# Optimization experiments

Measured on AMD Instinct MI355X. Metric: run time of the kernel, lower is better.

## Reference

```python
import jax, jax.numpy as jnp
import numpy as np

B, D = 16384, 1024

def setup_inputs() -> dict:
    key = jax.random.key(0)
    k1, k2, k3, k4 = jax.random.split(key, 4)
    return {
        "mu_q": jax.random.normal(k1, (B, D), dtype=jnp.float32),
        "sigma_q": jax.random.normal(k2, (B, D), dtype=jnp.float32),
        "mu_p": jax.random.normal(k3, (B, D), dtype=jnp.float32),
        "sigma_p": jax.random.normal(k4, (B, D), dtype=jnp.float32),
    }

def reference(mu_q, sigma_q, mu_p, sigma_p):
    # KL(p || q) for diagonal Gaussians where sigma_* are log-variances.
    # Matches torch.distributions.kl_divergence(MVN(mu_p, diag(exp(sigma_p))),
    #                                           MVN(mu_q, diag(exp(sigma_q)))).
    # Closed form per sample:
    #   0.5 * sum_d[ exp(sp - sq) + (mu_q - mu_p)^2 * exp(-sq) + sq - sp - 1 ]
    diff = mu_q - mu_p
    kl = 0.5 * jnp.sum(
        jnp.exp(sigma_p - sigma_q)
        + diff * diff * jnp.exp(-sigma_q)
        + sigma_q - sigma_p - 1.0,
        axis=-1,
    )
    return kl  # shape [B]
```

## Files before the change

### kernel.cpp

```cpp
#include <hip/hip_runtime.h>


constexpr int D_DIM = 1024;

typedef float f32x4 __attribute__((ext_vector_type(4)));

__global__ __launch_bounds__(256) void _KLD_MVNx2_kernel(
    const float* __restrict__ mu_q,
    const float* __restrict__ sigma_q,
    const float* __restrict__ mu_p,
    const float* __restrict__ sigma_p,
    float* __restrict__ out,
    int B)
{
    const int row = blockIdx.x;
    if (row >= B) return;
    const int tid = threadIdx.x;

    const size_t base = (size_t)row * D_DIM + (size_t)tid * 4;

    const f32x4 mq = __builtin_nontemporal_load(
        reinterpret_cast<const f32x4*>(mu_q + base));
    const f32x4 mp = __builtin_nontemporal_load(
        reinterpret_cast<const f32x4*>(mu_p + base));
    const f32x4 sq = *reinterpret_cast<const f32x4*>(sigma_q + base);
    const f32x4 sp = *reinterpret_cast<const f32x4*>(sigma_p + base);

    float s = 0.0f;
    #pragma unroll
    for (int j = 0; j < 4; ++j) {
        float d = mq[j] - mp[j];
        s += __expf(sp[j] - sq[j]) + d * d * __expf(-sq[j]) + (sq[j] - sp[j]);
    }
    s -= 4.0f;

    #pragma unroll
    for (int off = 32; off > 0; off >>= 1)
        s += __shfl_down(s, off);

    __shared__ float part[4];
    const int lane = tid & 63;
    const int wv   = tid >> 6;
    if (lane == 0) part[wv] = s;
    __syncthreads();

    if (tid == 0)
        out[row] = 0.5f * (part[0] + part[1] + part[2] + part[3]);
}

extern "C" void kernel_launch(void* const* d_in, const int* in_sizes, int n_in,
                              void* d_out, int out_size, void* d_ws, size_t ws_size,
                              hipStream_t stream) {
    const float* mu_q    = (const float*)d_in[0];
    const float* sigma_q = (const float*)d_in[1];
    const float* mu_p    = (const float*)d_in[2];
    const float* sigma_p = (const float*)d_in[3];
    float* out = (float*)d_out;

    const int B = out_size;
    _KLD_MVNx2_kernel<<<B, 256, 0, stream>>>(mu_q, sigma_q, mu_p, sigma_p, out, B);
}
```

Before: 43.26 us.

## Map one wavefront per row and drop shared-memory block reduction

Each 64-lane wavefront now processes a full 1024-element row with four f32x4 loads per input, and each 256-thread block handles four rows. The shared-memory partials and __syncthreads are gone, and each row is reduced entirely by wave shuffles. Nontemporal load hints are also removed. The goal is more bytes in flight per thread and less block-level sync, at the cost of higher register use per thread.

```diff
diff --git a/kernel.cpp b/kernel.cpp
--- a/kernel.cpp
+++ b/kernel.cpp
@@ -13,39 +13,41 @@
     float* __restrict__ out,
     int B)
 {
-    const int row = blockIdx.x;
+    const int wv   = threadIdx.x >> 6;
+    const int lane = threadIdx.x & 63;
+    const int row  = blockIdx.x * 4 + wv;
     if (row >= B) return;
-    const int tid = threadIdx.x;
 
-    const size_t base = (size_t)row * D_DIM + (size_t)tid * 4;
+    const size_t rb = (size_t)row * D_DIM;
 
-    const f32x4 mq = __builtin_nontemporal_load(
-        reinterpret_cast<const f32x4*>(mu_q + base));
-    const f32x4 mp = __builtin_nontemporal_load(
-        reinterpret_cast<const f32x4*>(mu_p + base));
-    const f32x4 sq = *reinterpret_cast<const f32x4*>(sigma_q + base);
-    const f32x4 sp = *reinterpret_cast<const f32x4*>(sigma_p + base);
+    f32x4 mq[4], sq[4], mp[4], sp[4];
+    #pragma unroll
+    for (int c = 0; c < 4; ++c) {
+        const size_t idx = rb + (size_t)c * 256 + (size_t)lane * 4;
+        mq[c] = *reinterpret_cast<const f32x4*>(mu_q    + idx);
+        mp[c] = *reinterpret_cast<const f32x4*>(mu_p    + idx);
+        sq[c] = *reinterpret_cast<const f32x4*>(sigma_q + idx);
+        sp[c] = *reinterpret_cast<const f32x4*>(sigma_p + idx);
+    }
 
-    float s = 0.0f;
+    float s = -16.0f;
     #pragma unroll
-    for (int j = 0; j < 4; ++j) {
-        float d = mq[j] - mp[j];
-        s += __expf(sp[j] - sq[j]) + d * d * __expf(-sq[j]) + (sq[j] - sp[j]);
+    for (int c = 0; c < 4; ++c) {
+        #pragma unroll
+        for (int j = 0; j < 4; ++j) {
+            const float d = mq[c][j] - mp[c][j];
+            s += __expf(sp[c][j] - sq[c][j])
+               + d * d * __expf(-sq[c][j])
+               + (sq[c][j] - sp[c][j]);
+        }
     }
-    s -= 4.0f;
 
     #pragma unroll
     for (int off = 32; off > 0; off >>= 1)
         s += __shfl_down(s, off);
 
-    __shared__ float part[4];
-    const int lane = tid & 63;
-    const int wv   = tid >> 6;
-    if (lane == 0) part[wv] = s;
-    __syncthreads();
-
-    if (tid == 0)
-        out[row] = 0.5f * (part[0] + part[1] + part[2] + part[3]);
+    if (lane == 0)
+        out[row] = 0.5f * s;
 }
 
 extern "C" void kernel_launch(void* const* d_in, const int* in_sizes, int n_in,
@@ -58,5 +60,6 @@
     float* out = (float*)d_out;
 
     const int B = out_size;
-    _KLD_MVNx2_kernel<<<B, 256, 0, stream>>>(mu_q, sigma_q, mu_p, sigma_p, out, B);
+    const int blocks = (B + 3) / 4;
+    _KLD_MVNx2_kernel<<<blocks, 256, 0, stream>>>(mu_q, sigma_q, mu_p, sigma_p, out, B);
 }
```

Result: faster. 42.37 us (-2.1%).
